# Kernel tuning notes

Hardware: AMD Instinct MI355X
Metric: run time of the kernel (lower is better)

The kernel has to match this reference:

```python
import jax, jax.numpy as jnp
import numpy as np


def table_operator(A, B):
    # A, B: (size, batch). Returns (16, size, batch) of soft logic-gate outputs.
    AB = A * B
    A_or_B = A + B - AB
    A_xor_B = A + B - 2.0 * AB
    return jnp.stack([
        jnp.zeros_like(A),          # 0: FALSE
        AB,                         # 1: A AND B
        A - AB,                     # 2: A AND NOT B
        A,                          # 3: A
        B - AB,                     # 4: NOT A AND B
        B,                          # 5: B
        A_xor_B,                    # 6: A XOR B
        A_or_B,                     # 7: A OR B
        1.0 - A_or_B,               # 8: NOR
        1.0 - A_xor_B,              # 9: XNOR
        1.0 - B,                    # 10: NOT B
        1.0 - B + AB,               # 11: B -> A
        1.0 - A,                    # 12: NOT A
        1.0 - A + AB,               # 13: A -> B
        1.0 - AB,                   # 14: NAND
        jnp.ones_like(A),           # 15: TRUE
    ], axis=0)


def setup_inputs() -> dict:
    key = jax.random.key(0)
    k1, k2, k3, k4 = jax.random.split(key, 4)
    prev_size, size, batch = 1024, 1024, 16384
    return {
        "prev_layer_output": jax.random.uniform(k1, (prev_size, batch), jnp.float32),
        "input_A_weights": jax.random.normal(k2, (size, prev_size), jnp.float32),
        "input_B_weights": jax.random.normal(k3, (size, prev_size), jnp.float32),
        "table_weights": jax.random.normal(k4, (16, size), jnp.float32),
    }


def reference(prev_layer_output, input_A_weights, input_B_weights, table_weights):
    # Inference path (torch.is_grad_enabled() == False, drop_out_rate == 0):
    # plain softmaxes, no multiplier shift, no dropout. GradFactor is identity in fwd.
    pA = jax.nn.softmax(input_A_weights, axis=1)   # (size, prev_size)
    pB = jax.nn.softmax(input_B_weights, axis=1)
    pT = jax.nn.softmax(table_weights, axis=0)     # (16, size)
    a = pA @ prev_layer_output                     # (size, batch)
    b = pB @ prev_layer_output                     # (size, batch)
    gates = table_operator(a, b)                   # (16, size, batch)
    return jnp.sum(gates * pT[:, :, None], axis=0)  # (size, batch)
```

## Files before the change

kernel.cpp:

```cpp
#include <hip/hip_runtime.h>
#include <hip/hip_bf16.h>


typedef __attribute__((ext_vector_type(8))) short bf16x8;
typedef __attribute__((ext_vector_type(4))) float f32x4;

__device__ __forceinline__ void gload_lds16(const void* g, void* l) {
    __builtin_amdgcn_global_load_lds(
        (const __attribute__((address_space(1))) void*)g,
        (__attribute__((address_space(3))) void*)l, 16, 0, 0);
}

__global__ __launch_bounds__(256) void softmax_rows_bf16(
    const float* __restrict__ WA, const float* __restrict__ WB,
    __hip_bfloat16* __restrict__ PA, __hip_bfloat16* __restrict__ PB,
    int rows, int cols)
{
    const int b = blockIdx.x;
    const float* W;
    __hip_bfloat16* P;
    if (b < rows) { W = WA + (size_t)b * cols;          P = PA + (size_t)b * cols; }
    else          { W = WB + (size_t)(b - rows) * cols; P = PB + (size_t)(b - rows) * cols; }

    const int t = threadIdx.x;
    const int wave = t >> 6, lane = t & 63;

    float4 v = *(const float4*)&W[t * 4];
    float mx = fmaxf(fmaxf(v.x, v.y), fmaxf(v.z, v.w));
    #pragma unroll
    for (int off = 32; off; off >>= 1) mx = fmaxf(mx, __shfl_xor(mx, off));

    __shared__ float redmax[4];
    __shared__ float redsum[4];
    if (lane == 0) redmax[wave] = mx;
    __syncthreads();
    mx = fmaxf(fmaxf(redmax[0], redmax[1]), fmaxf(redmax[2], redmax[3]));

    float e0 = __expf(v.x - mx), e1 = __expf(v.y - mx);
    float e2 = __expf(v.z - mx), e3 = __expf(v.w - mx);
    float s = e0 + e1 + e2 + e3;
    #pragma unroll
    for (int off = 32; off; off >>= 1) s += __shfl_xor(s, off);
    if (lane == 0) redsum[wave] = s;
    __syncthreads();
    s = redsum[0] + redsum[1] + redsum[2] + redsum[3];

    const float inv = 1.0f / s;
    __align__(8) __hip_bfloat16 o[4];
    o[0] = __float2bfloat16(e0 * inv);
    o[1] = __float2bfloat16(e1 * inv);
    o[2] = __float2bfloat16(e2 * inv);
    o[3] = __float2bfloat16(e3 * inv);
    *(uint2*)&P[t * 4] = *(const uint2*)o;
}

__global__ void table_coef(const float* __restrict__ TW, float4* __restrict__ coef, int size)
{
    const int s = blockIdx.x * blockDim.x + threadIdx.x;
    if (s >= size) return;
    float p[16];
    float mx = -1e30f;
    #pragma unroll
    for (int g = 0; g < 16; ++g) { p[g] = TW[g * size + s]; mx = fmaxf(mx, p[g]); }
    float sum = 0.f;
    #pragma unroll
    for (int g = 0; g < 16; ++g) { p[g] = __expf(p[g] - mx); sum += p[g]; }
    const float inv = 1.0f / sum;
    #pragma unroll
    for (int g = 0; g < 16; ++g) p[g] *= inv;

    float w0  = p[8] + p[9] + p[10] + p[11] + p[12] + p[13] + p[14] + p[15];
    float wA  = p[2] + p[3] + p[6] + p[7] - p[8] - p[9] - p[12] - p[13];
    float wB  = p[4] + p[5] + p[6] + p[7] - p[8] - p[9] - p[10] - p[11];
    float wAB = p[1] - p[2] - p[4] - 2.f * p[6] - p[7]
              + p[8] + 2.f * p[9] + p[11] + p[13] - p[14];
    coef[s] = make_float4(w0, wA, wB, wAB);
}

__global__ __launch_bounds__(256) void transpose_bf16(
    const float* __restrict__ prev, __hip_bfloat16* __restrict__ prevT,
    int K, int N)
{
    __shared__ float ls[64][65];
    const int k0 = blockIdx.y * 64, n0 = blockIdx.x * 64;
    const int t = threadIdx.x;

    {
        const int kr = t >> 4, nc = (t & 15) * 4;
        #pragma unroll
        for (int i = 0; i < 4; ++i) {
            const int k = i * 16 + kr;
            float4 v = *(const float4*)&prev[(size_t)(k0 + k) * N + n0 + nc];
            ls[k][nc + 0] = v.x; ls[k][nc + 1] = v.y;
            ls[k][nc + 2] = v.z; ls[k][nc + 3] = v.w;
        }
    }
    __syncthreads();
    {
        const int n = t >> 2, kc = (t & 3) * 16;
        __align__(16) __hip_bfloat16 tmp[16];
        #pragma unroll
        for (int j = 0; j < 16; ++j) tmp[j] = __float2bfloat16(ls[kc + j][n]);
        __hip_bfloat16* dst = &prevT[(size_t)(n0 + n) * K + k0 + kc];
        *(uint4*)(dst + 0) = *(const uint4*)&tmp[0];
        *(uint4*)(dst + 8) = *(const uint4*)&tmp[8];
    }
}

__global__ __launch_bounds__(256, 2) void dual_gemm(
    const __hip_bfloat16* __restrict__ pA,
    const __hip_bfloat16* __restrict__ pB,
    const __hip_bfloat16* __restrict__ prevT,
    const float4* __restrict__ coef,
    float* __restrict__ out,
    int M, int N, int K)
{
    __shared__ __hip_bfloat16 sAa[128][32];
    __shared__ __hip_bfloat16 sAb[128][32];
    __shared__ __hip_bfloat16 sB [128][32];

    const int t = threadIdx.x;
    const int wave = t >> 6, lane = t & 63;
    const int wr = wave >> 1, wc = wave & 1;
    const int m0 = blockIdx.y * 128, n0 = blockIdx.x * 128;

    const int srow  = lane >> 2;
    const int scol8 = (lane & 3) * 8;

    const int fr = lane & 15;
    const int kg = lane >> 4;

    f32x4 acc_a[4][4] = {};
    f32x4 acc_b[4][4] = {};

    for (int k0 = 0; k0 < K; k0 += 32) {
        __syncthreads();
        #pragma unroll
        for (int i = 0; i < 2; ++i) {
            const int chunk = wave * 2 + i;
            const int row = chunk * 16 + srow;
            gload_lds16(&pA   [(size_t)(m0 + row) * K + k0 + scol8], &sAa[chunk * 16][0]);
            gload_lds16(&pB   [(size_t)(m0 + row) * K + k0 + scol8], &sAb[chunk * 16][0]);
            gload_lds16(&prevT[(size_t)(n0 + row) * K + k0 + scol8], &sB [chunk * 16][0]);
        }
        __syncthreads();

        bf16x8 fa[4], fb[4], fv[4];
        #pragma unroll
        for (int i = 0; i < 4; ++i) {
            fa[i] = *(const bf16x8*)&sAa[wr * 64 + i * 16 + fr][kg * 8];
            fb[i] = *(const bf16x8*)&sAb[wr * 64 + i * 16 + fr][kg * 8];
            fv[i] = *(const bf16x8*)&sB [wc * 64 + i * 16 + fr][kg * 8];
        }
        #pragma unroll
        for (int i = 0; i < 4; ++i) {
            #pragma unroll
            for (int j = 0; j < 4; ++j) {
                acc_a[i][j] = __builtin_amdgcn_mfma_f32_16x16x32_bf16(fa[i], fv[j], acc_a[i][j], 0, 0, 0);
                acc_b[i][j] = __builtin_amdgcn_mfma_f32_16x16x32_bf16(fb[i], fv[j], acc_b[i][j], 0, 0, 0);
            }
        }
    }

    #pragma unroll
    for (int i = 0; i < 4; ++i) {
        #pragma unroll
        for (int r = 0; r < 4; ++r) {
            const int m = m0 + wr * 64 + i * 16 + kg * 4 + r;
            const float4 c = coef[m];
            #pragma unroll
            for (int j = 0; j < 4; ++j) {
                const int n = n0 + wc * 64 + j * 16 + fr;
                const float a = acc_a[i][j][r];
                const float b = acc_b[i][j][r];
                out[(size_t)m * N + n] = c.x + c.y * a + c.z * b + c.w * (a * b);
            }
        }
    }
}

extern "C" void kernel_launch(void* const* d_in, const int* in_sizes, int n_in,
                              void* d_out, int out_size, void* d_ws, size_t ws_size,
                              hipStream_t stream)
{
    const float* prev = (const float*)d_in[0];
    const float* WA   = (const float*)d_in[1];
    const float* WB   = (const float*)d_in[2];
    const float* TW   = (const float*)d_in[3];
    float* out = (float*)d_out;

    const int size      = in_sizes[3] / 16;
    const int prev_size = in_sizes[1] / size;
    const int batch     = in_sizes[0] / prev_size;

    char* ws = (char*)d_ws;
    __hip_bfloat16* prevT = (__hip_bfloat16*)ws;
    size_t off = (size_t)batch * prev_size * sizeof(__hip_bfloat16);
    __hip_bfloat16* pA = (__hip_bfloat16*)(ws + off);
    off += (size_t)size * prev_size * sizeof(__hip_bfloat16);
    __hip_bfloat16* pB = (__hip_bfloat16*)(ws + off);
    off += (size_t)size * prev_size * sizeof(__hip_bfloat16);
    float4* coef = (float4*)(ws + off);

    softmax_rows_bf16<<<dim3(2 * size), dim3(256), 0, stream>>>(
        WA, WB, pA, pB, size, prev_size);
    table_coef<<<dim3((size + 255) / 256), dim3(256), 0, stream>>>(TW, coef, size);
    transpose_bf16<<<dim3(batch / 64, prev_size / 64), dim3(256), 0, stream>>>(
        prev, prevT, prev_size, batch);
    dual_gemm<<<dim3(batch / 128, size / 128), dim3(256), 0, stream>>>(
        pA, pB, prevT, coef, out, size, batch, prev_size);
}
```

Baseline: 101.7 us.

## Rewrite dual GEMM with 8 waves, 4-stage LDS pipeline and swizzled layout

Replaces the single-buffered dual GEMM with a 512-thread kernel computing a 128x256 tile. It keeps a 4-deep ring of LDS buffers filled by direct global-to-LDS loads, XOR-swizzles the LDS layout to avoid bank conflicts, and uses explicit waitcnt, barriers and setprio to overlap loads with MFMA. Waves split the A and B products (wr selects pA or pB), and the results are combined through LDS in the epilogue. The dimensions K and N are now hardcoded, and 128KB of LDS is used per block.

After: 95.44 us. 6.2% less time.

```diff
diff --git a/kernel.cpp b/kernel.cpp
--- a/kernel.cpp
+++ b/kernel.cpp
@@ -107,73 +107,140 @@
     }
 }
 
-__global__ __launch_bounds__(256, 2) void dual_gemm(
+constexpr int BK_   = 32;
+constexpr int NTIL  = 32;
+constexpr int BUF   = 32768;
+constexpr int BOFF_ = 16384;
+constexpr int Kd    = 1024;
+constexpr int Nd    = 16384;
+
+__global__ __launch_bounds__(512, 2) void dual_gemm8(
     const __hip_bfloat16* __restrict__ pA,
     const __hip_bfloat16* __restrict__ pB,
     const __hip_bfloat16* __restrict__ prevT,
     const float4* __restrict__ coef,
-    float* __restrict__ out,
-    int M, int N, int K)
-{
-    __shared__ __hip_bfloat16 sAa[128][32];
-    __shared__ __hip_bfloat16 sAb[128][32];
-    __shared__ __hip_bfloat16 sB [128][32];
+    float* __restrict__ out)
+{
+    __shared__ __align__(16) char smem[131072];
 
     const int t = threadIdx.x;
     const int wave = t >> 6, lane = t & 63;
-    const int wr = wave >> 1, wc = wave & 1;
-    const int m0 = blockIdx.y * 128, n0 = blockIdx.x * 128;
-
-    const int srow  = lane >> 2;
-    const int scol8 = (lane & 3) * 8;
-
-    const int fr = lane & 15;
-    const int kg = lane >> 4;
-
-    f32x4 acc_a[4][4] = {};
-    f32x4 acc_b[4][4] = {};
-
-    for (int k0 = 0; k0 < K; k0 += 32) {
-        __syncthreads();
-        #pragma unroll
-        for (int i = 0; i < 2; ++i) {
-            const int chunk = wave * 2 + i;
-            const int row = chunk * 16 + srow;
-            gload_lds16(&pA   [(size_t)(m0 + row) * K + k0 + scol8], &sAa[chunk * 16][0]);
-            gload_lds16(&pB   [(size_t)(m0 + row) * K + k0 + scol8], &sAb[chunk * 16][0]);
-            gload_lds16(&prevT[(size_t)(n0 + row) * K + k0 + scol8], &sB [chunk * 16][0]);
-        }
-        __syncthreads();
-
-        bf16x8 fa[4], fb[4], fv[4];
-        #pragma unroll
-        for (int i = 0; i < 4; ++i) {
-            fa[i] = *(const bf16x8*)&sAa[wr * 64 + i * 16 + fr][kg * 8];
-            fb[i] = *(const bf16x8*)&sAb[wr * 64 + i * 16 + fr][kg * 8];
-            fv[i] = *(const bf16x8*)&sB [wc * 64 + i * 16 + fr][kg * 8];
-        }
-        #pragma unroll
-        for (int i = 0; i < 4; ++i) {
+    const int wr = wave >> 2, wc = wave & 3;
+    const int m0 = blockIdx.y * 128;
+    const int n0 = blockIdx.x * 256;
+
+    const int fr  = lane & 15;
+    const int kg  = lane >> 4;
+    const int csw = ((kg ^ ((fr >> 1) & 3)) << 4);
+    const int aoff = (wr * 128 + fr) * 64 + csw;
+    const int boff = BOFF_ + (wc * 64 + fr) * 64 + csw;
+
+    const int srow = lane >> 2;
+    const int sksw = ((lane & 3) ^ ((lane >> 3) & 3)) * 8;
+    const int arow = 16 * wave + srow;
+    const __hip_bfloat16* gA0 = pA    + (size_t)(m0 + arow) * Kd + sksw;
+    const __hip_bfloat16* gA1 = pB    + (size_t)(m0 + arow) * Kd + sksw;
+    const __hip_bfloat16* gB0 = prevT + (size_t)(n0 + arow) * Kd + sksw;
+    const __hip_bfloat16* gB1 = prevT + (size_t)(n0 + 128 + arow) * Kd + sksw;
+
+    auto STAGE_A = [&](int T) {
+        char* base = smem + (T & 3) * BUF + wave * 1024;
+        const int kT = T * BK_;
+        gload_lds16(gA0 + kT, base);
+        gload_lds16(gA1 + kT, base + 8192);
+    };
+    auto STAGE_B = [&](int T) {
+        char* base = smem + (T & 3) * BUF + BOFF_ + wave * 1024;
+        const int kT = T * BK_;
+        gload_lds16(gB0 + kT, base);
+        gload_lds16(gB1 + kT, base + 8192);
+    };
+
+    f32x4 acc[8][4] = {};
+    bf16x8 af[8], bf_[4];
+
+#define PH_MFMA(I0)                                                         \
+    asm volatile("s_waitcnt lgkmcnt(0)" ::: "memory");                      \
+    __builtin_amdgcn_sched_barrier(0);                                      \
+    __builtin_amdgcn_s_setprio(1);                                          \
+    _Pragma("unroll")                                                       \
+    for (int i = (I0); i < (I0) + 4; ++i) {                                 \
+        _Pragma("unroll")                                                   \
+        for (int j = 0; j < 4; ++j)                                         \
+            acc[i][j] = __builtin_amdgcn_mfma_f32_16x16x32_bf16(            \
+                af[i], bf_[j], acc[i][j], 0, 0, 0);                         \
+    }                                                                       \
+    __builtin_amdgcn_s_setprio(0);
+
+#define DO_TILE(TT, STG, VMSTR)                                             \
+  {                                                                         \
+    const char* buf = smem + ((TT) & 3) * BUF;                              \
+    _Pragma("unroll")                                                       \
+    for (int i = 0; i < 4; ++i)                                             \
+        af[i] = *(const bf16x8*)(buf + aoff + i * 1024);                    \
+    _Pragma("unroll")                                                       \
+    for (int j = 0; j < 4; ++j)                                             \
+        bf_[j] = *(const bf16x8*)(buf + boff + j * 1024);                   \
+    if (STG) STAGE_A((TT) + 3);                                             \
+    __builtin_amdgcn_s_barrier();                                           \
+    PH_MFMA(0)                                                              \
+    __builtin_amdgcn_s_barrier();                                           \
+    _Pragma("unroll")                                                       \
+    for (int i = 4; i < 8; ++i)                                             \
+        af[i] = *(const bf16x8*)(buf + aoff + i * 1024);                    \
+    if (STG) STAGE_B((TT) + 3);                                             \
+    asm volatile("s_waitcnt " VMSTR ::: "memory");                          \
+    __builtin_amdgcn_s_barrier();                                           \
+    PH_MFMA(4)                                                              \
+    __builtin_amdgcn_s_barrier();                                           \
+  }
+
+    STAGE_A(0); STAGE_B(0);
+    STAGE_A(1); STAGE_B(1);
+    STAGE_A(2); STAGE_B(2);
+    asm volatile("s_waitcnt vmcnt(8)" ::: "memory");
+    __builtin_amdgcn_s_barrier();
+
+    for (int tt = 0; tt < NTIL - 3; ++tt) {
+        DO_TILE(tt, 1, "vmcnt(8)")
+    }
+    DO_TILE(NTIL - 3, 0, "vmcnt(4)")
+    DO_TILE(NTIL - 2, 0, "vmcnt(0)")
+    DO_TILE(NTIL - 1, 0, "vmcnt(0)")
+
+#undef DO_TILE
+#undef PH_MFMA
+
+    __syncthreads();
+    if (wr == 1) {
+        #pragma unroll
+        for (int i = 0; i < 8; ++i) {
             #pragma unroll
             for (int j = 0; j < 4; ++j) {
-                acc_a[i][j] = __builtin_amdgcn_mfma_f32_16x16x32_bf16(fa[i], fv[j], acc_a[i][j], 0, 0, 0);
-                acc_b[i][j] = __builtin_amdgcn_mfma_f32_16x16x32_bf16(fb[i], fv[j], acc_b[i][j], 0, 0, 0);
+                const int off = ((((wc * 8 + i) * 4 + j) * 64) + lane) * 16;
+                *(f32x4*)(smem + off) = acc[i][j];
             }
         }
     }
-
-    #pragma unroll
-    for (int i = 0; i < 4; ++i) {
-        #pragma unroll
-        for (int r = 0; r < 4; ++r) {
-            const int m = m0 + wr * 64 + i * 16 + kg * 4 + r;
-            const float4 c = coef[m];
+    __syncthreads();
+    if (wr == 0) {
+        const int hi = lane >> 4;
+        #pragma unroll
+        for (int i = 0; i < 8; ++i) {
+            float4 cc[4];
+            #pragma unroll
+            for (int r = 0; r < 4; ++r) cc[r] = coef[m0 + i * 16 + hi * 4 + r];
             #pragma unroll
             for (int j = 0; j < 4; ++j) {
+                const f32x4 bb = *(const f32x4*)(smem + ((((wc * 8 + i) * 4 + j) * 64) + lane) * 16);
                 const int n = n0 + wc * 64 + j * 16 + fr;
-                const float a = acc_a[i][j][r];
-                const float b = acc_b[i][j][r];
-                out[(size_t)m * N + n] = c.x + c.y * a + c.z * b + c.w * (a * b);
+                #pragma unroll
+                for (int r = 0; r < 4; ++r) {
+                    const int m = m0 + i * 16 + hi * 4 + r;
+                    const float a = acc[i][j][r];
+                    out[(size_t)m * Nd + n] = cc[r].x + cc[r].y * a + cc[r].z * bb[r]
+                                            + cc[r].w * (a * bb[r]);
+                }
             }
         }
     }
@@ -207,6 +274,6 @@
     table_coef<<<dim3((size + 255) / 256), dim3(256), 0, stream>>>(TW, coef, size);
     transpose_bf16<<<dim3(batch / 64, prev_size / 64), dim3(256), 0, stream>>>(
         prev, prevT, prev_size, batch);
-    dual_gemm<<<dim3(batch / 128, size / 128), dim3(256), 0, stream>>>(
-        pA, pB, prevT, coef, out, size, batch, prev_size);
-}
+    dual_gemm8<<<dim3(batch / 256, size / 128), dim3(512), 0, stream>>>(
+        pA, pB, prevT, coef, out);
+}
```

## Rewrite dual GEMM as 8-wave pipelined kernel with swizzled LDS and split A/B waves

Applied to the files above, without the earlier changes.

Replaces the simple 128x128 dual GEMM with a 512-thread kernel on 128x256 tiles. The K step grows to 64, LDS is double-buffered with XOR swizzling, loads are issued asynchronously and interleaved with MFMA phases using explicit waitcnt, barriers and setprio. Waves split so one half computes the pA product and the other the pB product, then combine through LDS for the gate epilogue. The aim is to overlap global loads with matrix math and cut LDS bank conflicts. In exchange, dimensions are hardcoded (K=1024, N=16384), the kernel uses 128KB of LDS, and the manual scheduling is fragile.

Result: faster. 91.29 us (-10.2%).

```diff
diff --git a/kernel.cpp b/kernel.cpp
--- a/kernel.cpp
+++ b/kernel.cpp
@@ -107,73 +107,150 @@
     }
 }
 
-__global__ __launch_bounds__(256, 2) void dual_gemm(
+constexpr int Kd = 1024;
+constexpr int Nd = 16384;
+
+__global__ __launch_bounds__(512, 2) void dual_gemm8(
     const __hip_bfloat16* __restrict__ pA,
     const __hip_bfloat16* __restrict__ pB,
     const __hip_bfloat16* __restrict__ prevT,
     const float4* __restrict__ coef,
-    float* __restrict__ out,
-    int M, int N, int K)
-{
-    __shared__ __hip_bfloat16 sAa[128][32];
-    __shared__ __hip_bfloat16 sAb[128][32];
-    __shared__ __hip_bfloat16 sB [128][32];
-
-    const int t = threadIdx.x;
-    const int wave = t >> 6, lane = t & 63;
-    const int wr = wave >> 1, wc = wave & 1;
-    const int m0 = blockIdx.y * 128, n0 = blockIdx.x * 128;
-
-    const int srow  = lane >> 2;
-    const int scol8 = (lane & 3) * 8;
-
-    const int fr = lane & 15;
-    const int kg = lane >> 4;
-
-    f32x4 acc_a[4][4] = {};
-    f32x4 acc_b[4][4] = {};
-
-    for (int k0 = 0; k0 < K; k0 += 32) {
-        __syncthreads();
-        #pragma unroll
-        for (int i = 0; i < 2; ++i) {
-            const int chunk = wave * 2 + i;
-            const int row = chunk * 16 + srow;
-            gload_lds16(&pA   [(size_t)(m0 + row) * K + k0 + scol8], &sAa[chunk * 16][0]);
-            gload_lds16(&pB   [(size_t)(m0 + row) * K + k0 + scol8], &sAb[chunk * 16][0]);
-            gload_lds16(&prevT[(size_t)(n0 + row) * K + k0 + scol8], &sB [chunk * 16][0]);
-        }
-        __syncthreads();
-
-        bf16x8 fa[4], fb[4], fv[4];
-        #pragma unroll
-        for (int i = 0; i < 4; ++i) {
-            fa[i] = *(const bf16x8*)&sAa[wr * 64 + i * 16 + fr][kg * 8];
-            fb[i] = *(const bf16x8*)&sAb[wr * 64 + i * 16 + fr][kg * 8];
-            fv[i] = *(const bf16x8*)&sB [wc * 64 + i * 16 + fr][kg * 8];
-        }
-        #pragma unroll
-        for (int i = 0; i < 4; ++i) {
+    float* __restrict__ out)
+{
+    __shared__ __align__(16) char smem[131072];
+
+    const int t_ = threadIdx.x;
+    const int wave = t_ >> 6, lane = t_ & 63;
+    const int wr = wave >> 2, wc = wave & 3;
+    const int m0 = blockIdx.y * 128;
+    const int n0 = blockIdx.x * 256;
+
+    const int fr  = lane & 15;
+    const int kg  = lane >> 4;
+    const int fsw = fr & 7;
+    const int c0 = (kg ^ fsw) * 16;
+    const int c1 = ((4 + kg) ^ fsw) * 16;
+    const int aoffs = (wr * 128 + fr) * 128;
+    const int boffs = 32768 + (wc * 64 + fr) * 128;
+
+    const int sr  = lane >> 3;
+    const int swz = ((lane & 7) ^ sr) * 8;
+    const int r0  = wave * 16 + sr;
+    const __hip_bfloat16* gA0 = pA    + (size_t)(m0 + r0) * Kd + swz;
+    const __hip_bfloat16* gA1 = pB    + (size_t)(m0 + r0) * Kd + swz;
+    const __hip_bfloat16* gB0 = prevT + (size_t)(n0 + r0) * Kd + swz;
+    const __hip_bfloat16* gB1 = prevT + (size_t)(n0 + 128 + r0) * Kd + swz;
+
+    f32x4 acc[8][4] = {};
+    bf16x8 a[8], b[8];
+
+#define STG(GP, BB, HOFF, KT) {                                             \
+    char* lb = smem + (BB) + (HOFF) + wave * 2048;                          \
+    gload_lds16((GP) + (KT), lb);                                           \
+    gload_lds16((GP) + (KT) + 8 * Kd, lb + 1024); }
+
+#define RD_ALO(BB) _Pragma("unroll") for (int i = 0; i < 4; ++i) {          \
+    a[i*2]   = *(const bf16x8*)(smem + (BB) + aoffs + i * 2048 + c0);       \
+    a[i*2+1] = *(const bf16x8*)(smem + (BB) + aoffs + i * 2048 + c1); }
+#define RD_AHI(BB) _Pragma("unroll") for (int i = 0; i < 4; ++i) {          \
+    a[i*2]   = *(const bf16x8*)(smem + (BB) + aoffs + 8192 + i * 2048 + c0);\
+    a[i*2+1] = *(const bf16x8*)(smem + (BB) + aoffs + 8192 + i * 2048 + c1); }
+#define RD_BLO(BB) _Pragma("unroll") for (int j = 0; j < 2; ++j) {          \
+    b[j*2]   = *(const bf16x8*)(smem + (BB) + boffs + j * 2048 + c0);       \
+    b[j*2+1] = *(const bf16x8*)(smem + (BB) + boffs + j * 2048 + c1); }
+#define RD_BHI(BB) _Pragma("unroll") for (int j = 0; j < 2; ++j) {          \
+    b[4+j*2]   = *(const bf16x8*)(smem + (BB) + boffs + 4096 + j * 2048 + c0); \
+    b[4+j*2+1] = *(const bf16x8*)(smem + (BB) + boffs + 4096 + j * 2048 + c1); }
+
+#define BAR __builtin_amdgcn_s_barrier()
+#define VMW(S) asm volatile("s_waitcnt " S ::: "memory")
+
+#define MM(I0, J0, BB0)                                                     \
+    asm volatile("s_waitcnt lgkmcnt(0)" ::: "memory");                      \
+    __builtin_amdgcn_sched_barrier(0);                                      \
+    __builtin_amdgcn_s_setprio(1);                                          \
+    _Pragma("unroll") for (int i = 0; i < 4; ++i)                           \
+    _Pragma("unroll") for (int j = 0; j < 2; ++j)                           \
+    _Pragma("unroll") for (int ks = 0; ks < 2; ++ks)                        \
+        acc[(I0)+i][(J0)+j] = __builtin_amdgcn_mfma_f32_16x16x32_bf16(      \
+            a[i*2+ks], b[(BB0)+j*2+ks], acc[(I0)+i][(J0)+j], 0, 0, 0);      \
+    __builtin_amdgcn_s_setprio(0);
+
+#define TILE(T, CURB, NXTB, SA, SB, VM1) {                                  \
+    RD_ALO(CURB) RD_BLO(CURB)                                               \
+    if (SA) STG(gA0, NXTB, 0, ((T)+1)*64)                                   \
+    asm volatile("s_waitcnt lgkmcnt(8)" ::: "memory");                      \
+    VMW(VM1); BAR;                                                          \
+    MM(0, 0, 0) BAR;                                                        \
+    RD_BHI(CURB)                                                            \
+    if (SA) STG(gA1, NXTB, 16384, ((T)+1)*64)                               \
+    VMW("vmcnt(6)"); BAR;                                                   \
+    MM(0, 2, 4) BAR;                                                        \
+    RD_AHI(CURB)                                                            \
+    if (SB) STG(gB0, CURB, 32768, ((T)+2)*64)                               \
+    VMW("vmcnt(6)"); BAR;                                                   \
+    MM(4, 2, 4) BAR;                                                        \
+    if (SB) STG(gB1, CURB, 49152, ((T)+2)*64)                               \
+    VMW("vmcnt(6)"); BAR;                                                   \
+    MM(4, 0, 0) BAR;                                                        \
+}
+
+    STG(gB0, 0, 32768, 0)
+    STG(gB1, 0, 49152, 0)
+    STG(gA0, 0, 0,     0)
+    STG(gA1, 0, 16384, 0)
+    STG(gB0, 65536, 32768, 64)
+    STG(gB1, 65536, 49152, 64)
+    VMW("vmcnt(4)");
+    BAR;
+
+    for (int t = 0; t < 14; t += 2) {
+        TILE(t,     0,     65536, 1, 1, "vmcnt(6)")
+        TILE(t + 1, 65536, 0,     1, 1, "vmcnt(6)")
+    }
+    TILE(14, 0,     65536, 1, 0, "vmcnt(6)")
+    TILE(15, 65536, 0,     0, 0, "vmcnt(0)")
+
+#undef TILE
+#undef MM
+#undef STG
+#undef RD_ALO
+#undef RD_AHI
+#undef RD_BLO
+#undef RD_BHI
+#undef BAR
+#undef VMW
+
+    __syncthreads();
+    if (wr == 1) {
+        #pragma unroll
+        for (int i = 0; i < 8; ++i) {
             #pragma unroll
             for (int j = 0; j < 4; ++j) {
-                acc_a[i][j] = __builtin_amdgcn_mfma_f32_16x16x32_bf16(fa[i], fv[j], acc_a[i][j], 0, 0, 0);
-                acc_b[i][j] = __builtin_amdgcn_mfma_f32_16x16x32_bf16(fb[i], fv[j], acc_b[i][j], 0, 0, 0);
+                const int off = ((((wc * 8 + i) * 4 + j) * 64) + lane) * 16;
+                *(f32x4*)(smem + off) = acc[i][j];
             }
         }
     }
-
-    #pragma unroll
-    for (int i = 0; i < 4; ++i) {
-        #pragma unroll
-        for (int r = 0; r < 4; ++r) {
-            const int m = m0 + wr * 64 + i * 16 + kg * 4 + r;
-            const float4 c = coef[m];
+    __syncthreads();
+    if (wr == 0) {
+        const int hi = lane >> 4;
+        #pragma unroll
+        for (int i = 0; i < 8; ++i) {
+            float4 cc[4];
+            #pragma unroll
+            for (int r = 0; r < 4; ++r) cc[r] = coef[m0 + i * 16 + hi * 4 + r];
             #pragma unroll
             for (int j = 0; j < 4; ++j) {
+                const f32x4 bb = *(const f32x4*)(smem + ((((wc * 8 + i) * 4 + j) * 64) + lane) * 16);
                 const int n = n0 + wc * 64 + j * 16 + fr;
-                const float a = acc_a[i][j][r];
-                const float b = acc_b[i][j][r];
-                out[(size_t)m * N + n] = c.x + c.y * a + c.z * b + c.w * (a * b);
+                #pragma unroll
+                for (int r = 0; r < 4; ++r) {
+                    const int m = m0 + i * 16 + hi * 4 + r;
+                    const float aa = acc[i][j][r];
+                    out[(size_t)m * Nd + n] = cc[r].x + cc[r].y * aa + cc[r].z * bb[r]
+                                            + cc[r].w * (aa * bb[r]);
+                }
             }
         }
     }
@@ -207,6 +284,6 @@
     table_coef<<<dim3((size + 255) / 256), dim3(256), 0, stream>>>(TW, coef, size);
     transpose_bf16<<<dim3(batch / 64, prev_size / 64), dim3(256), 0, stream>>>(
         prev, prevT, prev_size, batch);
-    dual_gemm<<<dim3(batch / 128, size / 128), dim3(256), 0, stream>>>(
-        pA, pB, prevT, coef, out, size, batch, prev_size);
-}
+    dual_gemm8<<<dim3(batch / 256, size / 128), dim3(512), 0, stream>>>(
+        pA, pB, prevT, coef, out);
+}
```
